# Optimization experiments

Measured on AMD Instinct MI355X. Metric: run time of the kernel, lower is better.

The kernel has to match this reference:

```python
import jax, jax.numpy as jnp
import numpy as np

WS, STRIDE, GRID, HW = 3, 2, 4, 9          # window, stride, 4x4 windows, 9x9 grid
HEADS, HEAD_DIM, DIM = 4, 16, 64
INNER = HEADS * HEAD_DIM                    # 64
BATCH = 8192

_RI = (np.arange(GRID) * STRIDE)[:, None] + np.arange(WS)[None, :]   # [4,3] row/col starts+offsets
_coords = np.array([[x, y] for x in range(WS) for y in range(WS)])   # [9,2]
_REL = (_coords[None, :, :] - _coords[:, None, :]) + (WS - 1)        # [9,9,2] in [0,4]


def setup_inputs() -> dict:
    key = jax.random.key(0)
    ks = jax.random.split(key, 6)
    return {
        "x": jax.random.normal(ks[0], (BATCH, HW, HW, DIM), jnp.float32),
        "w_qkv": jax.random.normal(ks[1], (3 * INNER, DIM), jnp.float32) * 0.05,
        "pos_embedding": jax.random.normal(ks[2], (2 * WS - 1, 2 * WS - 1), jnp.float32),
        "w1": jax.random.normal(ks[3], (DIM // 2, INNER), jnp.float32) * 0.05,
        "b1": jnp.zeros((DIM // 2,), jnp.float32),
        "ln_g": jnp.ones((DIM // 2,), jnp.float32),
        "ln_b": jnp.zeros((DIM // 2,), jnp.float32),
        "w2": jax.random.normal(ks[4], (DIM, DIM // 2), jnp.float32) * 0.05,
        "b2": jnp.zeros((DIM,), jnp.float32),
    }


def reference(x, w_qkv, pos_embedding, w1, b1, ln_g, ln_b, w2, b2):
    b = x.shape[0]
    ri = jnp.asarray(_RI)                                  # [4,3]
    rel0 = jnp.asarray(_REL[..., 0]); rel1 = jnp.asarray(_REL[..., 1])

    qkv = jnp.einsum('bhwc,oc->bhwo', x, w_qkv)            # [b,9,9,3*INNER]
    # nn.Unfold(k=3, s=2): overlapping 3x3 windows -> [b,4,4,3,3,3I] -> [b,16,9,3I]
    win = qkv[:, ri[:, None, :, None], ri[None, :, None, :], :]
    win = win.reshape(b, GRID * GRID, WS * WS, 3 * INNER)
    q, k, v = jnp.split(win, 3, axis=-1)

    def to_heads(t):  # [b,n,wh,(h d)] -> [b,h,n,wh,d]
        return t.reshape(b, GRID * GRID, WS * WS, HEADS, HEAD_DIM).transpose(0, 3, 1, 2, 4)
    q, k, v = to_heads(q), to_heads(k), to_heads(v)

    bias = pos_embedding[rel0, rel1]                       # [9,9] relative-position bias
    attn = jnp.einsum('bhwid,bhwjd->bhwij', q, k) * (HEAD_DIM ** -0.5) + bias
    attn = jax.nn.softmax(attn, axis=-1)
    out = jnp.einsum('bhwij,bhwjd->bhwid', attn, v)        # [b,H,16,9,D]

    # rearrange 'b h n wh d -> b (wh h d) n'
    outf = out.transpose(0, 3, 1, 4, 2).reshape(b, WS * WS * INNER, GRID * GRID)
    # nn.Fold interprets channels as (c, kernel_pos) with c = idx // 9; overlaps are summed
    tmp = outf.reshape(b, INNER, WS, WS, GRID, GRID).transpose(0, 4, 5, 2, 3, 1)  # [b,wi,wj,ki,kj,C]
    canvas = jnp.zeros((b, HW, HW, INNER), out.dtype)
    canvas = canvas.at[:, ri[:, None, :, None], ri[None, :, None, :], :].add(tmp)

    h1 = jnp.einsum('bhwc,oc->bhwo', canvas, w1) + b1      # Linear(inner, dim/2)
    mu = jnp.mean(h1, -1, keepdims=True)
    var = jnp.var(h1, -1, keepdims=True)
    h1 = (h1 - mu) * jax.lax.rsqrt(var + 1e-5) * ln_g + ln_b
    h1 = jax.nn.gelu(h1, approximate=False)                # torch nn.GELU default = exact erf
    return jnp.einsum('bhwc,oc->bhwo', h1, w2) + b2        # [b,9,9,DIM]
```

## Files before the change

kernel.cpp:

```cpp
#include <hip/hip_runtime.h>
#include <math.h>

#define BLOCK_ 512
#define BPB_   8
#define NBLK_  (8192/BPB_)

typedef __bf16 bf16x8 __attribute__((ext_vector_type(8)));
typedef float  f32x4  __attribute__((ext_vector_type(4)));
typedef unsigned short us8 __attribute__((ext_vector_type(8)));

#define XS_  72
#define QKS_ 136
#define VS_  72
#define CS_  68
#define W1S_ 72
#define W2S_ 40
#define HGS_ 40

struct alignas(16) Smem {
    unsigned short Xb[81*XS_];
    unsigned short QK[81*QKS_];
    unsigned short Vf[81*VS_];
    float          Cv[81*CS_];
    unsigned short W1[32*W1S_];
    unsigned short W2[64*W2S_];
    float Bias[81];
    float B1v[32], LnG[32], LnB[32], B2v[64];
};

__device__ __forceinline__ unsigned short f2bf(float f) {
    union { float f; unsigned u; } v; v.f = f;
    unsigned r = v.u + 0x7FFFu + ((v.u >> 16) & 1u);
    return (unsigned short)(r >> 16);
}
__device__ __forceinline__ float bf2f(unsigned short b) {
    union { float f; unsigned u; } v; v.u = ((unsigned)b) << 16;
    return v.f;
}
__device__ __forceinline__ us8 pack8(float4 a, float4 b) {
    us8 r;
    r[0]=f2bf(a.x); r[1]=f2bf(a.y); r[2]=f2bf(a.z); r[3]=f2bf(a.w);
    r[4]=f2bf(b.x); r[5]=f2bf(b.y); r[6]=f2bf(b.z); r[7]=f2bf(b.w);
    return r;
}
__device__ __forceinline__ us8 zero8() {
    us8 z;
    for (int e = 0; e < 8; ++e) z[e] = 0;
    return z;
}
__device__ __forceinline__ f32x4 zero4() {
    f32x4 z; z[0]=0.f; z[1]=0.f; z[2]=0.f; z[3]=0.f; return z;
}
__device__ __forceinline__ f32x4 mfma16(us8 a, us8 b, f32x4 c) {
    return __builtin_amdgcn_mfma_f32_16x16x32_bf16(
        __builtin_bit_cast(bf16x8, a), __builtin_bit_cast(bf16x8, b), c, 0, 0, 0);
}

__global__ __launch_bounds__(BLOCK_, 2)
void wattn_mfma(const float* __restrict__ x, const float* __restrict__ w_qkv,
                const float* __restrict__ pe, const float* __restrict__ w1,
                const float* __restrict__ b1, const float* __restrict__ lng,
                const float* __restrict__ lnb, const float* __restrict__ w2,
                const float* __restrict__ b2, float* __restrict__ out)
{
    __shared__ Smem sm;
    const int t = threadIdx.x;
    const int wv = t >> 6, lane = t & 63;
    const int lrow = lane & 15;
    const int g    = lane >> 4;
    const int lk   = g * 8;
    const int g4   = g * 4;
    const int ng = wv & 3, mg = wv >> 2;

    for (int task = t; task < 32*8; task += BLOCK_) {
        int p = task >> 3, c8 = task & 7;
        const float4* src = (const float4*)(w1 + p*64 + c8*8);
        *(us8*)&sm.W1[p*W1S_ + c8*8] = pack8(src[0], src[1]);
    }
    for (int task = t; task < 64*4; task += BLOCK_) {
        int p = task >> 2, c8 = task & 3;
        const float4* src = (const float4*)(w2 + p*32 + c8*8);
        *(us8*)&sm.W2[p*W2S_ + c8*8] = pack8(src[0], src[1]);
    }
    if (t < 32) { sm.B1v[t]=b1[t]; sm.LnG[t]=lng[t]; sm.LnB[t]=lnb[t]; }
    if (t >= 64 && t < 128) sm.B2v[t-64] = b2[t-64];
    if (t >= 128 && t < 209) {
        int ij = t-128; int i = ij/9, j = ij%9;
        sm.Bias[ij] = pe[((j/3)-(i/3)+2)*5 + ((j%3)-(i%3)+2)];
    }
    for (int idx = t; idx < 81*CS_; idx += BLOCK_) sm.Cv[idx] = 0.f;
    {
        const float* xb = x + (size_t)blockIdx.x * BPB_ * (81*64);
        for (int task = t; task < 648; task += BLOCK_) {
            int p = task >> 3, c8 = task & 7;
            const float4* src = (const float4*)(xb + p*64 + c8*8);
            *(us8*)&sm.Xb[p*XS_ + c8*8] = pack8(src[0], src[1]);
        }
    }
    __syncthreads();

    for (int bi = 0; bi < BPB_; ++bi) {
        const size_t b = (size_t)blockIdx.x * BPB_ + bi;
        const bool hasPF = (bi + 1 < BPB_);
        const bool hasPF2 = hasPF && (t < 136);

        {
            us8 af[3][2];
            #pragma unroll
            for (int mi = 0; mi < 3; ++mi) {
                const int arow = min(mg*48 + mi*16 + lrow, 80);
                #pragma unroll
                for (int k = 0; k < 2; ++k)
                    af[mi][k] = *(const us8*)&sm.Xb[arow*XS_ + k*32 + lk];
            }
            #pragma unroll
            for (int ni = 0; ni < 3; ++ni) {
                const int n = ng*3 + ni;
                us8 bq[2];
                #pragma unroll
                for (int k = 0; k < 2; ++k) {
                    const float4* src = (const float4*)(w_qkv + (n*16 + lrow)*64 + k*32 + lk);
                    bq[k] = pack8(src[0], src[1]);
                }
                f32x4 acc[3];
                #pragma unroll
                for (int mi = 0; mi < 3; ++mi) acc[mi] = zero4();
                #pragma unroll
                for (int k = 0; k < 2; ++k)
                    #pragma unroll
                    for (int mi = 0; mi < 3; ++mi)
                        acc[mi] = mfma16(af[mi][k], bq[k], acc[mi]);
                #pragma unroll
                for (int mi = 0; mi < 3; ++mi) {
                    const int row0 = mg*48 + mi*16 + g4;
                    if (n < 8) {
                        #pragma unroll
                        for (int r = 0; r < 4; ++r) {
                            int row = row0 + r;
                            if (row < 81) sm.QK[row*QKS_ + n*16 + lrow] = f2bf(acc[mi][r]);
                        }
                    } else {
                        #pragma unroll
                        for (int r = 0; r < 4; ++r) {
                            int row = row0 + r;
                            if (row < 81) sm.Vf[row*VS_ + (n-8)*16 + lrow] = f2bf(acc[mi][r]);
                        }
                    }
                }
            }
        }
        __syncthreads();

        #pragma unroll
        for (int u = 0; u < 8; ++u) {
            const int pp = (wv << 3) | u;
            const int w = pp >> 2, h = pp & 3;
            const int base = (w >> 2) * 18 + (w & 3) * 2;
            const int cc  = min(lrow, 8);
            const int pos = base + (cc/3)*9 + (cc - (cc/3)*3);
            us8 aK = zero8(), bQ = zero8();
            if (g < 2) {
                aK = *(const us8*)&sm.QK[pos*QKS_ + 64 + h*16 + lk];
                bQ = *(const us8*)&sm.QK[pos*QKS_ + h*16 + lk];
            }
            f32x4 s4 = mfma16(aK, bQ, zero4());
            const int ib = cc * 9;
            float raw[4];
            #pragma unroll
            for (int r = 0; r < 4; ++r) {
                int j = g4 + r;
                raw[r] = (j < 9) ? s4[r]*0.25f + sm.Bias[ib + j] : -1e30f;
            }
            float mx = fmaxf(fmaxf(raw[0], raw[1]), fmaxf(raw[2], raw[3]));
            mx = fmaxf(mx, __shfl_xor(mx, 16));
            mx = fmaxf(mx, __shfl_xor(mx, 32));
            float ex[4]; float sum = 0.f;
            #pragma unroll
            for (int r = 0; r < 4; ++r) { ex[r] = __expf(raw[r] - mx); sum += ex[r]; }
            sum += __shfl_xor(sum, 16);
            sum += __shfl_xor(sum, 32);
            const float inv = 1.f / sum;
            float pf[4];
            #pragma unroll
            for (int r = 0; r < 4; ++r) pf[r] = ex[r] * inv;
            float pg0 = __shfl_xor(pf[0], 16), pg1 = __shfl_xor(pf[1], 16);
            float pg2 = __shfl_xor(pf[2], 16), pg3 = __shfl_xor(pf[3], 16);
            float p8  = __shfl_xor(pf[0], 48);
            us8 a2 = zero8(), b2 = zero8();
            if (g == 0) {
                a2[0]=f2bf(pf[0]); a2[1]=f2bf(pf[1]); a2[2]=f2bf(pf[2]); a2[3]=f2bf(pf[3]);
                a2[4]=f2bf(pg0);  a2[5]=f2bf(pg1);  a2[6]=f2bf(pg2);  a2[7]=f2bf(pg3);
                const unsigned short* vb = &sm.Vf[base*VS_ + h*16 + lrow];
                b2[0]=vb[0];       b2[1]=vb[VS_];     b2[2]=vb[2*VS_];
                b2[3]=vb[9*VS_];   b2[4]=vb[10*VS_];  b2[5]=vb[11*VS_];
                b2[6]=vb[18*VS_];  b2[7]=vb[19*VS_];
            } else if (g == 1) {
                a2[0] = f2bf(p8);
                b2[0] = sm.Vf[(base+20)*VS_ + h*16 + lrow];
            }
            f32x4 o4 = mfma16(a2, b2, zero4());
            #pragma unroll
            for (int r = 0; r < 4; ++r) {
                int i = g4 + r;
                if (i < 9) {
                    int idx = i*64 + h*16 + lrow;
                    int c = idx/9, rr = idx - 9*c;
                    int row = base + (rr/3)*9 + (rr - (rr/3)*3);
                    atomicAdd(&sm.Cv[row*CS_ + c], o4[r]);
                }
            }
        }
        __syncthreads();

        float4 pA0, pA1, pB0, pB1;
        if (hasPF) {
            const float4* xn = (const float4*)(x + (b+1)*(81*64));
            pA0 = xn[t*2]; pA1 = xn[t*2+1];
            if (hasPF2) { pB0 = xn[(512+t)*2]; pB1 = xn[(512+t)*2+1]; }
        }

        if (wv < 6) {
            const int m = wv;
            const int arow = m*16 + lrow;
            us8 aF[2];
            #pragma unroll
            for (int k = 0; k < 2; ++k) {
                aF[k] = zero8();
                if (arow < 81) {
                    const float* cp = &sm.Cv[arow*CS_ + k*32 + lk];
                    aF[k] = pack8(*(const float4*)cp, *(const float4*)(cp+4));
                }
            }
            f32x4 a0 = zero4(), a1 = zero4();
            #pragma unroll
            for (int k = 0; k < 2; ++k) {
                us8 b0  = *(const us8*)&sm.W1[lrow*W1S_ + k*32 + lk];
                us8 b1f = *(const us8*)&sm.W1[(16+lrow)*W1S_ + k*32 + lk];
                a0 = mfma16(aF[k], b0, a0);
                a1 = mfma16(aF[k], b1f, a1);
            }
            float bb0 = sm.B1v[lrow], bb1 = sm.B1v[16+lrow];
            float gg0 = sm.LnG[lrow], gg1 = sm.LnG[16+lrow];
            float ee0 = sm.LnB[lrow], ee1 = sm.LnB[16+lrow];
            float v0[4], v1[4], srow[4], qrow[4];
            #pragma unroll
            for (int r=0;r<4;++r) {
                v0[r] = a0[r] + bb0; v1[r] = a1[r] + bb1;
                srow[r] = v0[r] + v1[r];
                qrow[r] = v0[r]*v0[r] + v1[r]*v1[r];
            }
            #pragma unroll
            for (int mask = 1; mask <= 8; mask <<= 1)
                #pragma unroll
                for (int r=0;r<4;++r) {
                    srow[r] += __shfl_xor(srow[r], mask);
                    qrow[r] += __shfl_xor(qrow[r], mask);
                }
            unsigned short* H1g = sm.QK;
            #pragma unroll
            for (int r=0;r<4;++r) {
                int row = m*16 + g4 + r;
                if (row < 81) {
                    float mean = srow[r]*(1.f/32.f);
                    float var  = qrow[r]*(1.f/32.f) - mean*mean;
                    float rs   = rsqrtf(var + 1e-5f);
                    float xn0 = (v0[r]-mean)*rs*gg0 + ee0;
                    float xn1 = (v1[r]-mean)*rs*gg1 + ee1;
                    float ge0 = 0.5f*xn0*(1.f + erff(xn0*0.70710678118654752f));
                    float ge1 = 0.5f*xn1*(1.f + erff(xn1*0.70710678118654752f));
                    H1g[row*HGS_ + lrow]      = f2bf(ge0);
                    H1g[row*HGS_ + 16 + lrow] = f2bf(ge1);
                }
            }
        }
        __syncthreads();

        {
            const unsigned short* H1g = sm.QK;
            #pragma unroll
            for (int ti = 0; ti < 3; ++ti) {
                int ft = wv*3 + ti;
                int m = ft >> 2, n = ft & 3;
                int arow = m*16 + lrow;
                us8 aH = zero8();
                if (arow < 81) aH = *(const us8*)&H1g[arow*HGS_ + lk];
                us8 bW = *(const us8*)&sm.W2[(n*16+lrow)*W2S_ + lk];
                f32x4 acc = mfma16(aH, bW, zero4());
                float bb = sm.B2v[n*16+lrow];
                int row0 = m*16 + g4;
                #pragma unroll
                for (int r=0;r<4;++r) {
                    int row = row0 + r;
                    if (row < 81)
                        out[(b*81 + (size_t)row)*64 + n*16 + lrow] = acc[r] + bb;
                }
            }
        }
        if (hasPF) {
            int p = t >> 3, c8 = t & 7;
            *(us8*)&sm.Xb[p*XS_ + c8*8] = pack8(pA0, pA1);
            if (hasPF2) {
                int task = 512 + t; p = task >> 3; c8 = task & 7;
                *(us8*)&sm.Xb[p*XS_ + c8*8] = pack8(pB0, pB1);
            }
        }
        for (int idx = t; idx < 81*CS_; idx += BLOCK_) sm.Cv[idx] = 0.f;
        __syncthreads();
    }
}

extern "C" void kernel_launch(void* const* d_in, const int* in_sizes, int n_in,
                              void* d_out, int out_size, void* d_ws, size_t ws_size,
                              hipStream_t stream) {
    const float* x     = (const float*)d_in[0];
    const float* w_qkv = (const float*)d_in[1];
    const float* pe    = (const float*)d_in[2];
    const float* w1    = (const float*)d_in[3];
    const float* b1    = (const float*)d_in[4];
    const float* lng   = (const float*)d_in[5];
    const float* lnb   = (const float*)d_in[6];
    const float* w2    = (const float*)d_in[7];
    const float* b2    = (const float*)d_in[8];
    float* outp = (float*)d_out;

    wattn_mfma<<<dim3(NBLK_), dim3(BLOCK_), 0, stream>>>(
        x, w_qkv, pe, w1, b1, lng, lnb, w2, b2, outp);
}
```

Before: 719.6 us.

## Split fused kernel into attention kernel and MLP kernel via global canvas

The single fused kernel becomes two. The first computes QKV and windowed attention and writes the folded canvas in fp32 to the output buffer. The second kernel, with one wave per batch element, reads the canvas back, applies the Linear, LayerNorm, GELU and Linear steps, and overwrites the buffer in place. The aim is to shrink shared memory and drop a block-wide barrier so the attention kernel gets better occupancy, at the cost of an extra round trip of roughly 170MB through global memory.

Measured after the change: 705.3 us. 1.02x faster.

```diff
diff --git a/kernel.cpp b/kernel.cpp
--- a/kernel.cpp
+++ b/kernel.cpp
@@ -4,6 +4,8 @@
 #define BLOCK_ 512
 #define BPB_   8
 #define NBLK_  (8192/BPB_)
+#define K2B_   256
+#define K2NBLK_ (8192/4)
 
 typedef __bf16 bf16x8 __attribute__((ext_vector_type(8)));
 typedef float  f32x4  __attribute__((ext_vector_type(4)));
@@ -11,20 +13,24 @@
 
 #define XS_  72
 #define QKS_ 136
-#define VS_  72
+#define VSK_ 68
 #define CS_  68
 #define W1S_ 72
 #define W2S_ 40
 #define HGS_ 40
 
-struct alignas(16) Smem {
+struct alignas(16) SmemK1 {
     unsigned short Xb[81*XS_];
     unsigned short QK[81*QKS_];
-    unsigned short Vf[81*VS_];
+    unsigned short Vf[81*VSK_];
     float          Cv[81*CS_];
+    float Bias[81];
+};
+
+struct alignas(16) SmemK2 {
     unsigned short W1[32*W1S_];
     unsigned short W2[64*W2S_];
-    float Bias[81];
+    unsigned short H1g[4][81*HGS_];
     float B1v[32], LnG[32], LnB[32], B2v[64];
 };
 
@@ -32,10 +38,6 @@
     union { float f; unsigned u; } v; v.f = f;
     unsigned r = v.u + 0x7FFFu + ((v.u >> 16) & 1u);
     return (unsigned short)(r >> 16);
-}
-__device__ __forceinline__ float bf2f(unsigned short b) {
-    union { float f; unsigned u; } v; v.u = ((unsigned)b) << 16;
-    return v.f;
 }
 __device__ __forceinline__ us8 pack8(float4 a, float4 b) {
     us8 r;
@@ -57,13 +59,10 @@
 }
 
 __global__ __launch_bounds__(BLOCK_, 2)
-void wattn_mfma(const float* __restrict__ x, const float* __restrict__ w_qkv,
-                const float* __restrict__ pe, const float* __restrict__ w1,
-                const float* __restrict__ b1, const float* __restrict__ lng,
-                const float* __restrict__ lnb, const float* __restrict__ w2,
-                const float* __restrict__ b2, float* __restrict__ out)
+void wattn_k1(const float* __restrict__ x, const float* __restrict__ w_qkv,
+              const float* __restrict__ pe, float* __restrict__ canvas)
 {
-    __shared__ Smem sm;
+    __shared__ SmemK1 sm;
     const int t = threadIdx.x;
     const int wv = t >> 6, lane = t & 63;
     const int lrow = lane & 15;
@@ -72,23 +71,10 @@
     const int g4   = g * 4;
     const int ng = wv & 3, mg = wv >> 2;
 
-    for (int task = t; task < 32*8; task += BLOCK_) {
-        int p = task >> 3, c8 = task & 7;
-        const float4* src = (const float4*)(w1 + p*64 + c8*8);
-        *(us8*)&sm.W1[p*W1S_ + c8*8] = pack8(src[0], src[1]);
-    }
-    for (int task = t; task < 64*4; task += BLOCK_) {
-        int p = task >> 2, c8 = task & 3;
-        const float4* src = (const float4*)(w2 + p*32 + c8*8);
-        *(us8*)&sm.W2[p*W2S_ + c8*8] = pack8(src[0], src[1]);
-    }
-    if (t < 32) { sm.B1v[t]=b1[t]; sm.LnG[t]=lng[t]; sm.LnB[t]=lnb[t]; }
-    if (t >= 64 && t < 128) sm.B2v[t-64] = b2[t-64];
     if (t >= 128 && t < 209) {
         int ij = t-128; int i = ij/9, j = ij%9;
         sm.Bias[ij] = pe[((j/3)-(i/3)+2)*5 + ((j%3)-(i%3)+2)];
     }
-    for (int idx = t; idx < 81*CS_; idx += BLOCK_) sm.Cv[idx] = 0.f;
     {
         const float* xb = x + (size_t)blockIdx.x * BPB_ * (81*64);
         for (int task = t; task < 648; task += BLOCK_) {
@@ -143,12 +129,13 @@
                         #pragma unroll
                         for (int r = 0; r < 4; ++r) {
                             int row = row0 + r;
-                            if (row < 81) sm.Vf[row*VS_ + (n-8)*16 + lrow] = f2bf(acc[mi][r]);
+                            if (row < 81) sm.Vf[row*VSK_ + (n-8)*16 + lrow] = f2bf(acc[mi][r]);
                         }
                     }
                 }
             }
         }
+        for (int idx = t; idx < 81*CS_; idx += BLOCK_) sm.Cv[idx] = 0.f;
         __syncthreads();
 
         #pragma unroll
@@ -190,13 +177,13 @@
             if (g == 0) {
                 a2[0]=f2bf(pf[0]); a2[1]=f2bf(pf[1]); a2[2]=f2bf(pf[2]); a2[3]=f2bf(pf[3]);
                 a2[4]=f2bf(pg0);  a2[5]=f2bf(pg1);  a2[6]=f2bf(pg2);  a2[7]=f2bf(pg3);
-                const unsigned short* vb = &sm.Vf[base*VS_ + h*16 + lrow];
-                b2[0]=vb[0];       b2[1]=vb[VS_];     b2[2]=vb[2*VS_];
-                b2[3]=vb[9*VS_];   b2[4]=vb[10*VS_];  b2[5]=vb[11*VS_];
-                b2[6]=vb[18*VS_];  b2[7]=vb[19*VS_];
+                const unsigned short* vb = &sm.Vf[base*VSK_ + h*16 + lrow];
+                b2[0]=vb[0];        b2[1]=vb[VSK_];     b2[2]=vb[2*VSK_];
+                b2[3]=vb[9*VSK_];   b2[4]=vb[10*VSK_];  b2[5]=vb[11*VSK_];
+                b2[6]=vb[18*VSK_];  b2[7]=vb[19*VSK_];
             } else if (g == 1) {
                 a2[0] = f2bf(p8);
-                b2[0] = sm.Vf[(base+20)*VS_ + h*16 + lrow];
+                b2[0] = sm.Vf[(base+20)*VSK_ + h*16 + lrow];
             }
             f32x4 o4 = mfma16(a2, b2, zero4());
             #pragma unroll
@@ -218,83 +205,10 @@
             pA0 = xn[t*2]; pA1 = xn[t*2+1];
             if (hasPF2) { pB0 = xn[(512+t)*2]; pB1 = xn[(512+t)*2+1]; }
         }
-
-        if (wv < 6) {
-            const int m = wv;
-            const int arow = m*16 + lrow;
-            us8 aF[2];
-            #pragma unroll
-            for (int k = 0; k < 2; ++k) {
-                aF[k] = zero8();
-                if (arow < 81) {
-                    const float* cp = &sm.Cv[arow*CS_ + k*32 + lk];
-                    aF[k] = pack8(*(const float4*)cp, *(const float4*)(cp+4));
-                }
-            }
-            f32x4 a0 = zero4(), a1 = zero4();
-            #pragma unroll
-            for (int k = 0; k < 2; ++k) {
-                us8 b0  = *(const us8*)&sm.W1[lrow*W1S_ + k*32 + lk];
-                us8 b1f = *(const us8*)&sm.W1[(16+lrow)*W1S_ + k*32 + lk];
-                a0 = mfma16(aF[k], b0, a0);
-                a1 = mfma16(aF[k], b1f, a1);
-            }
-            float bb0 = sm.B1v[lrow], bb1 = sm.B1v[16+lrow];
-            float gg0 = sm.LnG[lrow], gg1 = sm.LnG[16+lrow];
-            float ee0 = sm.LnB[lrow], ee1 = sm.LnB[16+lrow];
-            float v0[4], v1[4], srow[4], qrow[4];
-            #pragma unroll
-            for (int r=0;r<4;++r) {
-                v0[r] = a0[r] + bb0; v1[r] = a1[r] + bb1;
-                srow[r] = v0[r] + v1[r];
-                qrow[r] = v0[r]*v0[r] + v1[r]*v1[r];
-            }
-            #pragma unroll
-            for (int mask = 1; mask <= 8; mask <<= 1)
-                #pragma unroll
-                for (int r=0;r<4;++r) {
-                    srow[r] += __shfl_xor(srow[r], mask);
-                    qrow[r] += __shfl_xor(qrow[r], mask);
-                }
-            unsigned short* H1g = sm.QK;
-            #pragma unroll
-            for (int r=0;r<4;++r) {
-                int row = m*16 + g4 + r;
-                if (row < 81) {
-                    float mean = srow[r]*(1.f/32.f);
-                    float var  = qrow[r]*(1.f/32.f) - mean*mean;
-                    float rs   = rsqrtf(var + 1e-5f);
-                    float xn0 = (v0[r]-mean)*rs*gg0 + ee0;
-                    float xn1 = (v1[r]-mean)*rs*gg1 + ee1;
-                    float ge0 = 0.5f*xn0*(1.f + erff(xn0*0.70710678118654752f));
-                    float ge1 = 0.5f*xn1*(1.f + erff(xn1*0.70710678118654752f));
-                    H1g[row*HGS_ + lrow]      = f2bf(ge0);
-                    H1g[row*HGS_ + 16 + lrow] = f2bf(ge1);
-                }
-            }
-        }
-        __syncthreads();
-
-        {
-            const unsigned short* H1g = sm.QK;
-            #pragma unroll
-            for (int ti = 0; ti < 3; ++ti) {
-                int ft = wv*3 + ti;
-                int m = ft >> 2, n = ft & 3;
-                int arow = m*16 + lrow;
-                us8 aH = zero8();
-                if (arow < 81) aH = *(const us8*)&H1g[arow*HGS_ + lk];
-                us8 bW = *(const us8*)&sm.W2[(n*16+lrow)*W2S_ + lk];
-                f32x4 acc = mfma16(aH, bW, zero4());
-                float bb = sm.B2v[n*16+lrow];
-                int row0 = m*16 + g4;
-                #pragma unroll
-                for (int r=0;r<4;++r) {
-                    int row = row0 + r;
-                    if (row < 81)
-                        out[(b*81 + (size_t)row)*64 + n*16 + lrow] = acc[r] + bb;
-                }
-            }
+        for (int idx = t; idx < 81*16; idx += BLOCK_) {
+            int p = idx >> 4, c4 = idx & 15;
+            *(float4*)&canvas[(b*81 + (size_t)p)*64 + c4*4] =
+                *(const float4*)&sm.Cv[p*CS_ + c4*4];
         }
         if (hasPF) {
             int p = t >> 3, c8 = t & 7;
@@ -304,8 +218,109 @@
                 *(us8*)&sm.Xb[p*XS_ + c8*8] = pack8(pB0, pB1);
             }
         }
-        for (int idx = t; idx < 81*CS_; idx += BLOCK_) sm.Cv[idx] = 0.f;
         __syncthreads();
+    }
+}
+
+__global__ __launch_bounds__(K2B_, 4)
+void wattn_k2(float* __restrict__ io, const float* __restrict__ w1,
+              const float* __restrict__ b1, const float* __restrict__ lng,
+              const float* __restrict__ lnb, const float* __restrict__ w2,
+              const float* __restrict__ b2)
+{
+    __shared__ SmemK2 sm;
+    const int t = threadIdx.x;
+    const int wv = t >> 6, lane = t & 63;
+    const int lrow = lane & 15;
+    const int g    = lane >> 4;
+    const int lk   = g * 8;
+    const int g4   = g * 4;
+
+    for (int task = t; task < 32*8; task += K2B_) {
+        int p = task >> 3, c8 = task & 7;
+        const float4* src = (const float4*)(w1 + p*64 + c8*8);
+        *(us8*)&sm.W1[p*W1S_ + c8*8] = pack8(src[0], src[1]);
+    }
+    for (int task = t; task < 64*4; task += K2B_) {
+        int p = task >> 2, c8 = task & 3;
+        const float4* src = (const float4*)(w2 + p*32 + c8*8);
+        *(us8*)&sm.W2[p*W2S_ + c8*8] = pack8(src[0], src[1]);
+    }
+    if (t < 32) { sm.B1v[t]=b1[t]; sm.LnG[t]=lng[t]; sm.LnB[t]=lnb[t]; }
+    if (t >= 64 && t < 128) sm.B2v[t-64] = b2[t-64];
+    __syncthreads();
+
+    const size_t b = (size_t)blockIdx.x * 4 + wv;
+    float* canv = io + b * (81*64);
+    unsigned short* H1g = sm.H1g[wv];
+
+    const float bb0 = sm.B1v[lrow], bb1 = sm.B1v[16+lrow];
+    const float gg0 = sm.LnG[lrow], gg1 = sm.LnG[16+lrow];
+    const float ee0 = sm.LnB[lrow], ee1 = sm.LnB[16+lrow];
+
+    #pragma unroll
+    for (int m = 0; m < 6; ++m) {
+        const int arow = m*16 + lrow;
+        us8 aF[2];
+        #pragma unroll
+        for (int k = 0; k < 2; ++k) {
+            aF[k] = zero8();
+            if (arow < 81) {
+                const float* cp = canv + arow*64 + k*32 + lk;
+                aF[k] = pack8(*(const float4*)cp, *(const float4*)(cp+4));
+            }
+        }
+        f32x4 a0 = zero4(), a1 = zero4();
+        #pragma unroll
+        for (int k = 0; k < 2; ++k) {
+            us8 b0  = *(const us8*)&sm.W1[lrow*W1S_ + k*32 + lk];
+            us8 b1f = *(const us8*)&sm.W1[(16+lrow)*W1S_ + k*32 + lk];
+            a0 = mfma16(aF[k], b0, a0);
+            a1 = mfma16(aF[k], b1f, a1);
+        }
+        float v0[4], v1[4], srow[4], qrow[4];
+        #pragma unroll
+        for (int r=0;r<4;++r) {
+            v0[r] = a0[r] + bb0; v1[r] = a1[r] + bb1;
+            srow[r] = v0[r] + v1[r];
+            qrow[r] = v0[r]*v0[r] + v1[r]*v1[r];
+        }
+        #pragma unroll
+        for (int mask = 1; mask <= 8; mask <<= 1)
+            #pragma unroll
+            for (int r=0;r<4;++r) {
+                srow[r] += __shfl_xor(srow[r], mask);
+                qrow[r] += __shfl_xor(qrow[r], mask);
+            }
+        #pragma unroll
+        for (int r=0;r<4;++r) {
+            int row = m*16 + g4 + r;
+            if (row < 81) {
+                float mean = srow[r]*(1.f/32.f);
+                float var  = qrow[r]*(1.f/32.f) - mean*mean;
+                float rs   = rsqrtf(var + 1e-5f);
+                float xn0 = (v0[r]-mean)*rs*gg0 + ee0;
+                float xn1 = (v1[r]-mean)*rs*gg1 + ee1;
+                float ge0 = 0.5f*xn0*(1.f + erff(xn0*0.70710678118654752f));
+                float ge1 = 0.5f*xn1*(1.f + erff(xn1*0.70710678118654752f));
+                H1g[row*HGS_ + lrow]      = f2bf(ge0);
+                H1g[row*HGS_ + 16 + lrow] = f2bf(ge1);
+            }
+        }
+        us8 aH = zero8();
+        if (arow < 81) aH = *(const us8*)&H1g[arow*HGS_ + lk];
+        #pragma unroll
+        for (int n = 0; n < 4; ++n) {
+            us8 bW = *(const us8*)&sm.W2[(n*16+lrow)*W2S_ + lk];
+            f32x4 acc = mfma16(aH, bW, zero4());
+            float bb = sm.B2v[n*16+lrow];
+            #pragma unroll
+            for (int r=0;r<4;++r) {
+                int row = m*16 + g4 + r;
+                if (row < 81)
+                    canv[row*64 + n*16 + lrow] = acc[r] + bb;
+            }
+        }
     }
 }
 
@@ -323,6 +338,6 @@
     const float* b2    = (const float*)d_in[8];
     float* outp = (float*)d_out;
 
-    wattn_mfma<<<dim3(NBLK_), dim3(BLOCK_), 0, stream>>>(
-        x, w_qkv, pe, w1, b1, lng, lnb, w2, b2, outp);
-}
+    wattn_k1<<<dim3(NBLK_), dim3(BLOCK_), 0, stream>>>(x, w_qkv, pe, outp);
+    wattn_k2<<<dim3(K2NBLK_), dim3(K2B_), 0, stream>>>(outp, w1, b1, lng, lnb, w2, b2);
+}
```
